# Performance work log

Measured on AMD Instinct MI355X. Metric: run time of the kernel, lower is better.

Reference implementation:

```python
import jax, jax.numpy as jnp
import numpy as np

L_LAYERS = 6   # decoder layers
N_HEAD = 8
NUM_PAIR = 100  # num_pair_queries
LN_EPS = 1e-5


def _ln(x, g, b):
    m = x.mean(-1, keepdims=True)
    v = ((x - m) ** 2).mean(-1, keepdims=True)
    return (x - m) / jnp.sqrt(v + LN_EPS) * g + b


def _mlp2(x, w1, b1, w2, b2):
    return jax.nn.relu(x @ w1.T + b1) @ w2.T + b2


def _mha(q, k, v, in_w, in_b, out_w, out_b):
    # torch nn.MultiheadAttention (batch_first, eval mode) equivalent
    C = q.shape[-1]
    dh = C // N_HEAD
    wq, wk, wv = jnp.split(in_w, 3, axis=0)
    bq, bk, bv = jnp.split(in_b, 3, axis=0)
    def heads(x, w, b):
        y = x @ w.T + b
        return y.reshape(x.shape[0], x.shape[1], N_HEAD, dh).transpose(0, 2, 1, 3)
    qh, kh, vh = heads(q, wq, bq), heads(k, wk, bk), heads(v, wv, bv)
    att = jax.nn.softmax(jnp.einsum('bhqd,bhkd->bhqk', qh, kh) * (1.0 / np.sqrt(dh)), axis=-1)
    out = jnp.einsum('bhqk,bhkd->bhqd', att, vh).transpose(0, 2, 1, 3).reshape(q.shape[0], q.shape[1], C)
    return out @ out_w.T + out_b


def reference(hs_last, mem, mem_pos, sub_boxes, obj_boxes,
              su_w1, su_b1, su_w2, su_b2, ou_w1, ou_b1, ou_w2, ou_b2,
              pm_w1, pm_b1, pm_w2, pm_b2, sp_w1, sp_b1, sp_w2, sp_b2,
              sa_in_w, sa_in_b, sa_out_w, sa_out_b, ca_in_w, ca_in_b, ca_out_w, ca_out_b,
              l1_w, l1_b, l2_w, l2_b, n1_g, n1_b, n2_g, n2_b, n3_g, n3_b):
    B, Q, C = hs_last.shape
    N = Q // 2
    hsp = hs_last.reshape(B, N, 2, C)
    sub_feat, obj_feat = hsp[:, :, 0, :], hsp[:, :, 1, :]

    # --- HumanObjectPairLearner.select_topk_indices (mapper='identity') ---
    sub_emb = _mlp2(sub_feat, su_w1, su_b1, su_w2, su_b2)
    obj_emb = _mlp2(obj_feat, ou_w1, ou_b1, ou_w2, ou_b2)
    sub_emb = sub_emb / (jnp.linalg.norm(sub_emb, axis=-1, keepdims=True) + 1e-6)
    obj_emb = obj_emb / (jnp.linalg.norm(obj_emb, axis=-1, keepdims=True) + 1e-6)
    importance = jnp.einsum('bnc,bmc->bnm', sub_emb, obj_emb)  # [B, N, N]
    K = min(NUM_PAIR, N * N)
    _, idx = jax.lax.top_k(importance.reshape(B, N * N), K)
    sub_pos, obj_pos = idx // N, idx % N  # [B, K]

    # --- build_pair_queries: gather selected sub/obj features ---
    sel_sub = jnp.take_along_axis(sub_feat, sub_pos[:, :, None], axis=1)  # [B, K, C]
    sel_obj = jnp.take_along_axis(obj_feat, obj_pos[:, :, None], axis=1)
    pair_q = _mlp2(jnp.concatenate([sel_sub, sel_obj], axis=-1), pm_w1, pm_b1, pm_w2, pm_b2)

    # --- PairSpatialEncoding ---
    sp = _mlp2(jnp.concatenate([sub_boxes, obj_boxes], axis=-1), sp_w1, sp_b1, sp_w2, sp_b2)

    # --- LocalityAwareInteractionDecoder (eval mode: dropout = identity) ---
    q = pair_q
    k_mem = mem + mem_pos
    for i in range(L_LAYERS):
        q_sp = q + sp
        sa = _mha(q_sp, q_sp, q_sp, sa_in_w[i], sa_in_b[i], sa_out_w[i], sa_out_b[i])
        q = _ln(q + sa, n1_g[i], n1_b[i])
        # original: cross_attn(cat([q, sp], dim=1), ...)[:, :K] -- attention is
        # per-query, so slicing after equals running cross-attn with q alone.
        ca = _mha(q, k_mem, mem, ca_in_w[i], ca_in_b[i], ca_out_w[i], ca_out_b[i])
        q = _ln(q + ca, n2_g[i], n2_b[i])
        ffn = jax.nn.relu(q @ l1_w[i].T + l1_b[i]) @ l2_w[i].T + l2_b[i]
        q = _ln(q + ffn, n3_g[i], n3_b[i])
    return q


def setup_inputs() -> dict:
    B, N, C, M, F, L = 32, 100, 256, 4096, 2048, L_LAYERS
    K = NUM_PAIR
    keys = iter(jax.random.split(jax.random.key(0), 80))
    def nrm(shape, s=1.0):
        return jax.random.normal(next(keys), shape, jnp.float32) * s
    w = lambda shape: nrm(shape, 0.02)
    return {
        'hs_last': nrm((B, 2 * N, C)),
        'mem': nrm((B, M, C)),
        'mem_pos': nrm((B, M, C)),
        'sub_boxes': jax.random.uniform(next(keys), (B, K, 4), jnp.float32),
        'obj_boxes': jax.random.uniform(next(keys), (B, K, 4), jnp.float32),
        'su_w1': w((C, C)), 'su_b1': jnp.zeros((C,)), 'su_w2': w((C, C)), 'su_b2': jnp.zeros((C,)),
        'ou_w1': w((C, C)), 'ou_b1': jnp.zeros((C,)), 'ou_w2': w((C, C)), 'ou_b2': jnp.zeros((C,)),
        'pm_w1': w((C, 2 * C)), 'pm_b1': jnp.zeros((C,)), 'pm_w2': w((C, C)), 'pm_b2': jnp.zeros((C,)),
        'sp_w1': w((C, 8)), 'sp_b1': jnp.zeros((C,)), 'sp_w2': w((C, C)), 'sp_b2': jnp.zeros((C,)),
        'sa_in_w': w((L, 3 * C, C)), 'sa_in_b': jnp.zeros((L, 3 * C)),
        'sa_out_w': w((L, C, C)), 'sa_out_b': jnp.zeros((L, C)),
        'ca_in_w': w((L, 3 * C, C)), 'ca_in_b': jnp.zeros((L, 3 * C)),
        'ca_out_w': w((L, C, C)), 'ca_out_b': jnp.zeros((L, C)),
        'l1_w': w((L, F, C)), 'l1_b': jnp.zeros((L, F)),
        'l2_w': w((L, C, F)), 'l2_b': jnp.zeros((L, C)),
        'n1_g': jnp.ones((L, C)), 'n1_b': jnp.zeros((L, C)),
        'n2_g': jnp.ones((L, C)), 'n2_b': jnp.zeros((L, C)),
        'n3_g': jnp.ones((L, C)), 'n3_b': jnp.zeros((L, C)),
    }
```

## Files before the change

### kernel.cpp

```cpp
#include <hip/hip_runtime.h>
#include <hip/hip_bf16.h>

#define Bb 32
#define Nn 100
#define Cc 256
#define Mm 4096
#define Ff 2048
#define Ll 6
#define Hh 8
#define DH 32
#define KP 100
#define TT (Bb*KP)
#define LNEPS 1e-5f
#define NCH 4
#define SUBK 128

typedef __hip_bfloat16 bf16;
typedef unsigned short ushort_t;
typedef __attribute__((ext_vector_type(8))) short short8v;
typedef __attribute__((ext_vector_type(4))) float f32x4;

union FragU { uint2 u2[2]; uint4 u4; short8v s8; };

__device__ __forceinline__ float bfu2f(unsigned short u) {
  union { unsigned u32; float f; } cv; cv.u32 = ((unsigned)u) << 16; return cv.f;
}
__device__ __forceinline__ unsigned short f2bf(float f) {
  union { float f; unsigned u; } c; c.f = f;
  unsigned r = c.u + 0x7FFF + ((c.u >> 16) & 1);
  return (unsigned short)(r >> 16);
}
__device__ __forceinline__ unsigned pack2(float a, float b) {
  return (unsigned)f2bf(a) | ((unsigned)f2bf(b) << 16);
}

template<int AT, bool RELU, int OM, bool PAIR>
__global__ __launch_bounds__(256) void gemm_mfma(
    const void* __restrict__ Av, const float* __restrict__ A2,
    const bf16* __restrict__ W, const float* __restrict__ bias,
    void* __restrict__ out,
    const void* __restrict__ Av2, const float* __restrict__ A2_2,
    const bf16* __restrict__ W2, const float* __restrict__ bias2,
    void* __restrict__ out2,
    int M, int N, int K)
{
  __shared__ ushort_t SM[2*128*72];
  ushort_t* As = SM;
  ushort_t* Bs = SM + 128*72;
  const int mt = M >> 7, nt = N >> 7;
  const int nwg1 = mt * nt;
  const int nwg = PAIR ? 2*nwg1 : nwg1;
  const int g = blockIdx.x;
  const int xcd = g & 7, lid = g >> 3;
  const int q8 = nwg >> 3, r8 = nwg & 7;
  int wgid = (xcd < r8 ? xcd*(q8+1) : r8*(q8+1) + (xcd - r8)*q8) + lid;
  if (PAIR && wgid >= nwg1) {
    wgid -= nwg1; Av = Av2; A2 = A2_2; W = W2; bias = bias2; out = out2;
  }
  const int ntile = wgid % nt, mtile = wgid / nt;
  const int bm = mtile << 7, bn = ntile << 7;
  const int tid = threadIdx.x;
  const int w = tid >> 6, lane = tid & 63;
  const int lr = lane & 15, lg = lane >> 4;
  const int wm = w >> 1, wn = w & 1;
  const float* Af = (const float*)Av;
  const bf16*  Ab = (const bf16*)Av;

  f32x4 acc[4][4] = {};

  for (int k0 = 0; k0 < K; k0 += 64) {
    __syncthreads();
    #pragma unroll
    for (int i = 0; i < 4; ++i) {
      int linear = i*256 + tid;
      int row = linear >> 3, c8 = linear & 7;
      uint4 packed;
      if (AT == 0) {
        const float* ap = Af + (size_t)(bm+row)*K + k0 + c8*8;
        float4 f0 = *(const float4*)ap;
        float4 f1 = *(const float4*)(ap+4);
        if (A2) {
          const float* ap2 = A2 + (size_t)(bm+row)*K + k0 + c8*8;
          float4 g0 = *(const float4*)ap2;
          float4 g1 = *(const float4*)(ap2+4);
          f0.x += g0.x; f0.y += g0.y; f0.z += g0.z; f0.w += g0.w;
          f1.x += g1.x; f1.y += g1.y; f1.z += g1.z; f1.w += g1.w;
        }
        packed.x = pack2(f0.x, f0.y); packed.y = pack2(f0.z, f0.w);
        packed.z = pack2(f1.x, f1.y); packed.w = pack2(f1.z, f1.w);
      } else {
        packed = *(const uint4*)(Ab + (size_t)(bm+row)*K + k0 + c8*8);
      }
      *(uint4*)&As[row*72 + c8*8] = packed;
      uint4 wb = *(const uint4*)(W + (size_t)(bn+row)*K + k0 + c8*8);
      *(uint4*)&Bs[row*72 + c8*8] = wb;
    }
    __syncthreads();
    #pragma unroll
    for (int kk = 0; kk < 64; kk += 32) {
      FragU a[4];
      #pragma unroll
      for (int mi = 0; mi < 4; ++mi)
        a[mi].u4 = *(const uint4*)&As[(wm*64 + mi*16 + lr)*72 + kk + lg*8];
      #pragma unroll
      for (int ni = 0; ni < 4; ++ni) {
        FragU bfr;
        bfr.u4 = *(const uint4*)&Bs[(wn*64 + ni*16 + lr)*72 + kk + lg*8];
        #pragma unroll
        for (int mi = 0; mi < 4; ++mi)
          acc[mi][ni] = __builtin_amdgcn_mfma_f32_16x16x32_bf16(a[mi].s8, bfr.s8,
                                                                acc[mi][ni], 0, 0, 0);
      }
    }
  }

  if (OM == 2) {
    __syncthreads();
    ushort_t* Ct = SM;
    #pragma unroll
    for (int ni = 0; ni < 4; ++ni) {
      int col = wn*64 + ni*16 + lr;
      float bv = bias[bn + col];
      #pragma unroll
      for (int mi = 0; mi < 4; ++mi)
        #pragma unroll
        for (int r = 0; r < 4; ++r) {
          int rowl = wm*64 + mi*16 + lg*4 + r;
          Ct[rowl*136 + col] = f2bf(acc[mi][ni][r] + bv);
        }
    }
    __syncthreads();
    for (int u = tid; u < 2048; u += 256) {
      int rowl = u >> 4, sub = u & 15;
      uint4 v = *(const uint4*)&Ct[rowl*136 + sub*8];
      int m = bm + rowl;
      int gcol = bn + sub*8;
      int bb = m >> 12, mm = m & 4095;
      int h = gcol >> 5, dd = gcol & 31;
      *(uint4*)((bf16*)out + (((size_t)bb*Hh + h)*Mm + mm)*DH + dd) = v;
    }
  } else {
    #pragma unroll
    for (int ni = 0; ni < 4; ++ni) {
      int col = bn + wn*64 + ni*16 + lr;
      float bv = bias ? bias[col] : 0.f;
      #pragma unroll
      for (int mi = 0; mi < 4; ++mi) {
        #pragma unroll
        for (int r = 0; r < 4; ++r) {
          int m = bm + wm*64 + mi*16 + lg*4 + r;
          float v = acc[mi][ni][r] + bv;
          if (RELU) v = fmaxf(v, 0.f);
          if (OM == 0) {
            ((float*)out)[(size_t)m*N + col] = v;
          } else if (OM == 1) {
            ((bf16*)out)[(size_t)m*N + col] = __float2bfloat16(v);
          } else {
            int bb = m / KP, qq = m % KP;
            int h = col >> 5, dd = col & 31;
            ((bf16*)out)[(((size_t)bb*Hh + h)*KP + qq)*DH + dd] =
                __float2bfloat16(v * 0.17677669529663687f);
          }
        }
      }
    }
  }
}

template<int AT>
__global__ __launch_bounds__(512) void gemm_ln(
    const void* __restrict__ Av, const bf16* __restrict__ W,
    const float* __restrict__ bias, const float* __restrict__ resid,
    const float* __restrict__ gamma, const float* __restrict__ beta,
    float* __restrict__ out, int M, int K,
    const bf16* __restrict__ part, const float2* __restrict__ ml)
{
  __shared__ ushort_t As[16][72];
  __shared__ ushort_t Bs[256][72];
  __shared__ float redS[16][8];
  __shared__ float redQ[16][8];
  const int bm = blockIdx.x * 16;
  const int tid = threadIdx.x;
  const int w = tid >> 6, lane = tid & 63;
  const int lr = lane & 15, lg = lane >> 4;
  const float* Af = (const float*)Av;
  const bf16*  Ab = (const bf16*)Av;
  f32x4 acc[2] = {};

  for (int k0 = 0; k0 < K; k0 += 64) {
    __syncthreads();
    if (tid < 128) {
      int row = tid >> 3, c8 = tid & 7;
      uint4 packed;
      if (AT == 0) {
        const float* ap = Af + (size_t)(bm+row)*K + k0 + c8*8;
        float4 f0 = *(const float4*)ap;
        float4 f1 = *(const float4*)(ap+4);
        packed.x = pack2(f0.x, f0.y); packed.y = pack2(f0.z, f0.w);
        packed.z = pack2(f1.x, f1.y); packed.w = pack2(f1.z, f1.w);
      } else if (AT == 1) {
        packed = *(const uint4*)(Ab + (size_t)(bm+row)*K + k0 + c8*8);
      } else {
        int t = bm + row;
        int b = t / KP, q = t % KP;
        int ch0 = k0 + c8*8;
        int h = ch0 >> 5, d0 = ch0 & 31;
        int bh = b*Hh + h;
        float2 m0 = ml[((size_t)bh*NCH + 0)*KP + q];
        float2 m1 = ml[((size_t)bh*NCH + 1)*KP + q];
        float2 m2 = ml[((size_t)bh*NCH + 2)*KP + q];
        float2 m3 = ml[((size_t)bh*NCH + 3)*KP + q];
        float mm = fmaxf(fmaxf(m0.x, m1.x), fmaxf(m2.x, m3.x));
        float w0 = __expf(m0.x - mm), w1 = __expf(m1.x - mm);
        float w2 = __expf(m2.x - mm), w3 = __expf(m3.x - mm);
        float invL = 1.f / (m0.y*w0 + m1.y*w1 + m2.y*w2 + m3.y*w3);
        float o[8] = {};
        float wc[NCH] = { w0, w1, w2, w3 };
        #pragma unroll
        for (int c = 0; c < NCH; ++c) {
          uint4 pv = *(const uint4*)(part + (((size_t)bh*NCH + c)*KP + q)*DH + d0);
          const ushort_t* pe = (const ushort_t*)&pv;
          #pragma unroll
          for (int e = 0; e < 8; ++e) o[e] += wc[c] * bfu2f(pe[e]);
        }
        packed.x = pack2(o[0]*invL, o[1]*invL);
        packed.y = pack2(o[2]*invL, o[3]*invL);
        packed.z = pack2(o[4]*invL, o[5]*invL);
        packed.w = pack2(o[6]*invL, o[7]*invL);
      }
      *(uint4*)&As[row][c8*8] = packed;
    }
    #pragma unroll
    for (int i = 0; i < 4; ++i) {
      int linear = i*512 + tid;
      int row = linear >> 3, c8 = linear & 7;
      *(uint4*)&Bs[row][c8*8] = *(const uint4*)(W + (size_t)row*K + k0 + c8*8);
    }
    __syncthreads();
    #pragma unroll
    for (int kk = 0; kk < 64; kk += 32) {
      FragU a;
      a.u4 = *(const uint4*)&As[lr][kk + lg*8];
      #pragma unroll
      for (int ni = 0; ni < 2; ++ni) {
        FragU bfr;
        bfr.u4 = *(const uint4*)&Bs[w*32 + ni*16 + lr][kk + lg*8];
        acc[ni] = __builtin_amdgcn_mfma_f32_16x16x32_bf16(a.s8, bfr.s8, acc[ni], 0, 0, 0);
      }
    }
  }

  float x[2][4];
  #pragma unroll
  for (int r = 0; r < 4; ++r) {
    int row = bm + lg*4 + r;
    float s = 0.f, sq = 0.f;
    #pragma unroll
    for (int ni = 0; ni < 2; ++ni) {
      int col = w*32 + ni*16 + lr;
      float v = acc[ni][r] + bias[col] + resid[(size_t)row*Cc + col];
      x[ni][r] = v;
      s += v; sq += v*v;
    }
    #pragma unroll
    for (int m2 = 1; m2 < 16; m2 <<= 1) { s += __shfl_xor(s, m2); sq += __shfl_xor(sq, m2); }
    if (lr == 0) { redS[lg*4 + r][w] = s; redQ[lg*4 + r][w] = sq; }
  }
  __syncthreads();
  #pragma unroll
  for (int r = 0; r < 4; ++r) {
    int lrow = lg*4 + r;
    float ss = 0.f, sq = 0.f;
    #pragma unroll
    for (int j = 0; j < 8; ++j) { ss += redS[lrow][j]; sq += redQ[lrow][j]; }
    float mean = ss * (1.f/Cc);
    float var = sq * (1.f/Cc) - mean*mean;
    float inv = rsqrtf(var + LNEPS);
    #pragma unroll
    for (int ni = 0; ni < 2; ++ni) {
      int col = w*32 + ni*16 + lr;
      out[(size_t)(bm+lrow)*Cc + col] = (x[ni][r] - mean)*inv*gamma[col] + beta[col];
    }
  }
}

#define NSEG 8
struct CvtDesc {
  const float* src[NSEG];
  bf16* dst[NSEG];
  int n4[NSEG];
  int total4;
};
__global__ __launch_bounds__(256) void cvt_multi(CvtDesc d) {
  int stride = gridDim.x * blockDim.x;
  for (int i = blockIdx.x*256 + threadIdx.x; i < d.total4; i += stride) {
    int seg = 0, off = i;
    while (off >= d.n4[seg]) { off -= d.n4[seg]; ++seg; }
    float4 f = *(const float4*)(d.src[seg] + (size_t)off*4);
    uint2 p; p.x = pack2(f.x, f.y); p.y = pack2(f.z, f.w);
    *(uint2*)(d.dst[seg] + (size_t)off*4) = p;
  }
}

__global__ __launch_bounds__(256) void prep_mem(const float* __restrict__ mem,
                                                const float* __restrict__ mem_pos,
                                                bf16* __restrict__ kb, bf16* __restrict__ vb,
                                                int n16) {
  int i = blockIdx.x*256 + threadIdx.x;
  if (i >= n16) return;
  size_t base = (size_t)i * 16;
  float4 a[4], p[4];
  #pragma unroll
  for (int t = 0; t < 4; ++t) {
    a[t] = *(const float4*)(mem + base + t*4);
    p[t] = *(const float4*)(mem_pos + base + t*4);
  }
  #pragma unroll
  for (int h = 0; h < 2; ++h) {
    uint4 vv, kv;
    vv.x = pack2(a[2*h].x, a[2*h].y);     vv.y = pack2(a[2*h].z, a[2*h].w);
    vv.z = pack2(a[2*h+1].x, a[2*h+1].y); vv.w = pack2(a[2*h+1].z, a[2*h+1].w);
    kv.x = pack2(a[2*h].x + p[2*h].x,     a[2*h].y + p[2*h].y);
    kv.y = pack2(a[2*h].z + p[2*h].z,     a[2*h].w + p[2*h].w);
    kv.z = pack2(a[2*h+1].x + p[2*h+1].x, a[2*h+1].y + p[2*h+1].y);
    kv.w = pack2(a[2*h+1].z + p[2*h+1].z, a[2*h+1].w + p[2*h+1].w);
    *(uint4*)(vb + base + h*8) = vv;
    *(uint4*)(kb + base + h*8) = kv;
  }
}

template<bool RELU>
__global__ __launch_bounds__(256) void gemm_nt(
    const float* __restrict__ A0, const float* __restrict__ W0,
    const float* __restrict__ b0, float* __restrict__ o0,
    const float* __restrict__ A1, const float* __restrict__ W1,
    const float* __restrict__ b1, float* __restrict__ o1,
    int M, int N, int K)
{
  const float* A = blockIdx.z ? A1 : A0;
  const float* Wt = blockIdx.z ? W1 : W0;
  const float* bias = blockIdx.z ? b1 : b0;
  float* out = blockIdx.z ? o1 : o0;
  __shared__ float As[16][68];
  __shared__ float Ws[16][68];
  const int bm = blockIdx.y * 64, bn = blockIdx.x * 64;
  const int tid = threadIdx.x;
  const int kk = tid & 15, rr = tid >> 4;
  const int tx = tid & 15, ty = tid >> 4;
  float acc[4][4] = {};
  for (int k0 = 0; k0 < K; k0 += 16) {
    #pragma unroll
    for (int p = 0; p < 4; ++p) {
      int m = rr + p*16;
      int row = bm + m;
      float av = 0.f, wv = 0.f;
      bool kin = (k0 + kk) < K;
      if (row < M && kin) av = A[(size_t)row * K + k0 + kk];
      int wrow = bn + m;
      if (wrow < N && kin) wv = Wt[(size_t)wrow * K + k0 + kk];
      As[kk][m] = av;
      Ws[kk][m] = wv;
    }
    __syncthreads();
    #pragma unroll
    for (int q = 0; q < 16; ++q) {
      float a[4], w[4];
      #pragma unroll
      for (int i = 0; i < 4; ++i) a[i] = As[q][ty*4 + i];
      #pragma unroll
      for (int j = 0; j < 4; ++j) w[j] = Ws[q][tx*4 + j];
      #pragma unroll
      for (int i = 0; i < 4; ++i)
        #pragma unroll
        for (int j = 0; j < 4; ++j) acc[i][j] += a[i] * w[j];
    }
    __syncthreads();
  }
  #pragma unroll
  for (int i = 0; i < 4; ++i) {
    int row = bm + ty*4 + i;
    if (row >= M) continue;
    #pragma unroll
    for (int j = 0; j < 4; ++j) {
      int col = bn + tx*4 + j;
      if (col >= N) continue;
      float v = acc[i][j];
      if (bias) v += bias[col];
      if (RELU) v = v > 0.f ? v : 0.f;
      out[(size_t)row*N + col] = v;
    }
  }
}

__global__ void split_subobj(const float* __restrict__ hs,
                             float* __restrict__ subf, float* __restrict__ objf) {
  int i = blockIdx.x*256 + threadIdx.x;
  if (i >= Bb*Nn*Cc) return;
  int c = i % Cc, n = (i / Cc) % Nn, b = i / (Cc*Nn);
  subf[i] = hs[((size_t)b*2*Nn + 2*n    )*Cc + c];
  objf[i] = hs[((size_t)b*2*Nn + 2*n + 1)*Cc + c];
}

__global__ __launch_bounds__(256) void l2norm_kernel(float* __restrict__ x) {
  int t = blockIdx.x, c = threadIdx.x;
  float v = x[(size_t)t*Cc + c];
  __shared__ float red[256];
  red[c] = v*v; __syncthreads();
  for (int s = 128; s > 0; s >>= 1) { if (c < s) red[c] += red[c+s]; __syncthreads(); }
  float scale = 1.f / (sqrtf(red[0]) + 1e-6f);
  x[(size_t)t*Cc + c] = v * scale;
}

__global__ __launch_bounds__(128) void importance_kernel(const float* __restrict__ se,
                                                         const float* __restrict__ oe,
                                                         float* __restrict__ imp) {
  int b = blockIdx.x / Nn, n = blockIdx.x % Nn;
  int m = threadIdx.x;
  if (m >= Nn) return;
  const float* s = se + ((size_t)b*Nn + n)*Cc;
  const float* o = oe + ((size_t)b*Nn + m)*Cc;
  float acc = 0.f;
  for (int c = 0; c < Cc; ++c) acc += s[c] * o[c];
  imp[((size_t)b*Nn + n)*Nn + m] = acc;
}

__global__ __launch_bounds__(1024) void topk_kernel(const float* __restrict__ imp,
                                                    int* __restrict__ idx_out) {
  __shared__ unsigned mu[Nn*Nn];
  __shared__ unsigned hist[256];
  __shared__ unsigned prefix;
  __shared__ int remK;
  __shared__ unsigned long long keys[128];
  __shared__ unsigned tiebuf[256];
  __shared__ unsigned cnt_gt, cnt_tie;
  const int b = blockIdx.x, tid = threadIdx.x;
  const int NN = Nn*Nn;

  for (int i = tid; i < NN; i += 1024) {
    unsigned u = __float_as_uint(imp[(size_t)b*NN + i]);
    mu[i] = (u & 0x80000000u) ? ~u : (u | 0x80000000u);
  }
  if (tid == 0) { prefix = 0u; remK = KP; cnt_gt = 0u; cnt_tie = 0u; }
  __syncthreads();

  for (int shift = 24; shift >= 0; shift -= 8) {
    if (tid < 256) hist[tid] = 0u;
    __syncthreads();
    unsigned pmask = (shift == 24) ? 0u : (0xFFFFFFFFu << (shift + 8));
    unsigned pref = prefix;
    for (int i = tid; i < NN; i += 1024) {
      unsigned v = mu[i];
      if ((v & pmask) == pref) atomicAdd(&hist[(v >> shift) & 0xFFu], 1u);
    }
    __syncthreads();
    if (tid == 0) {
      int rk = remK;
      unsigned sel = 0u;
      for (int bin = 255; bin >= 0; --bin) {
        int c = (int)hist[bin];
        if (c >= rk) { sel = (unsigned)bin; break; }
        rk -= c;
      }
      remK = rk;
      prefix = pref | (sel << shift);
    }
    __syncthreads();
  }

  const unsigned T = prefix;
  const int need = remK;

  for (int i = tid; i < NN; i += 1024) {
    unsigned v = mu[i];
    if (v > T) {
      unsigned p = atomicAdd(&cnt_gt, 1u);
      keys[p] = ((unsigned long long)(~v) << 32) | (unsigned)i;
    } else if (v == T) {
      unsigned p = atomicAdd(&cnt_tie, 1u);
      if (p < 256u) tiebuf[p] = (unsigned)i;
    }
  }
  __syncthreads();
  const unsigned ngt = cnt_gt;
  const unsigned nt_ = cnt_tie < 256u ? cnt_tie : 256u;

  for (int i = tid; i < 256; i += 1024) if (i >= (int)nt_) tiebuf[i] = 0xFFFFFFFFu;
  __syncthreads();
  for (int ksz = 2; ksz <= 256; ksz <<= 1) {
    for (int st = ksz >> 1; st > 0; st >>= 1) {
      if (tid < 128) {
        int i = ((tid & ~(st-1)) << 1) | (tid & (st-1));
        int j = i | st;
        bool up = ((i & ksz) == 0);
        unsigned a = tiebuf[i], c = tiebuf[j];
        if ((a > c) == up) { tiebuf[i] = c; tiebuf[j] = a; }
      }
      __syncthreads();
    }
  }
  for (int t = tid; t < need; t += 1024)
    keys[ngt + t] = ((unsigned long long)(~T) << 32) | tiebuf[t];
  for (int i = tid; i < 128; i += 1024)
    if (i >= KP) keys[i] = 0xFFFFFFFFFFFFFFFFull;
  __syncthreads();

  for (int ksz = 2; ksz <= 128; ksz <<= 1) {
    for (int st = ksz >> 1; st > 0; st >>= 1) {
      if (tid < 64) {
        int i = ((tid & ~(st-1)) << 1) | (tid & (st-1));
        int j = i | st;
        bool up = ((i & ksz) == 0);
        unsigned long long a = keys[i], c = keys[j];
        if ((a > c) == up) { keys[i] = c; keys[j] = a; }
      }
      __syncthreads();
    }
  }
  if (tid < KP) idx_out[b*KP + tid] = (int)(keys[tid] & 0xFFFFFFFFu);
}

__global__ __launch_bounds__(256) void gather_pair(const float* __restrict__ subf,
                                                   const float* __restrict__ objf,
                                                   const int* __restrict__ idx,
                                                   float* __restrict__ pc) {
  int bk = blockIdx.x;
  int b = bk / KP;
  int id = idx[bk];
  int spos = id / Nn, opos = id % Nn;
  const float* s = subf + ((size_t)b*Nn + spos)*Cc;
  const float* o = objf + ((size_t)b*Nn + opos)*Cc;
  float* dst = pc + (size_t)bk * (2*Cc);
  for (int c = threadIdx.x; c < Cc; c += 256) { dst[c] = s[c]; dst[Cc + c] = o[c]; }
}

__global__ void boxes_cat_kernel(const float* __restrict__ sb, const float* __restrict__ ob,
                                 float* __restrict__ out) {
  int i = blockIdx.x*256 + threadIdx.x;
  if (i >= TT*8) return;
  int c = i & 7, bk = i >> 3;
  out[i] = (c < 4) ? sb[bk*4 + c] : ob[bk*4 + (c - 4)];
}

__global__ __launch_bounds__(512) void attn_sa(const bf16* __restrict__ qkv,
                                               float* __restrict__ out) {
  __shared__ float Kt[128][36];
  __shared__ float Vt[128][36];
  __shared__ float Qs[KP][DH];
  __shared__ float Ps[8][128];
  int bh = blockIdx.x; int b = bh >> 3, h = bh & 7;
  int tid = threadIdx.x;
  const float scale = 0.17677669529663687f;
  const size_t base = (size_t)b * KP * (3*Cc);
  for (int i = tid; i < KP*DH; i += 512) {
    int q = i >> 5, d = i & 31;
    Qs[q][d] = __bfloat162float(qkv[base + (size_t)q*(3*Cc) + h*DH + d]) * scale;
  }
  {
    int j = tid >> 2, qc = tid & 3;
    float kf[8], vf[8];
    if (j < KP) {
      uint4 kraw = *(const uint4*)(qkv + base + (size_t)j*(3*Cc) + Cc   + h*DH + qc*8);
      uint4 vraw = *(const uint4*)(qkv + base + (size_t)j*(3*Cc) + 2*Cc + h*DH + qc*8);
      const ushort_t* ks = (const ushort_t*)&kraw;
      const ushort_t* vs = (const ushort_t*)&vraw;
      #pragma unroll
      for (int e = 0; e < 8; ++e) { kf[e] = bfu2f(ks[e]); vf[e] = bfu2f(vs[e]); }
    } else {
      #pragma unroll
      for (int e = 0; e < 8; ++e) { kf[e] = 0.f; vf[e] = 0.f; }
    }
    ((float4*)Kt[j])[qc*2]   = make_float4(kf[0],kf[1],kf[2],kf[3]);
    ((float4*)Kt[j])[qc*2+1] = make_float4(kf[4],kf[5],kf[6],kf[7]);
    ((float4*)Vt[j])[qc*2]   = make_float4(vf[0],vf[1],vf[2],vf[3]);
    ((float4*)Vt[j])[qc*2+1] = make_float4(vf[4],vf[5],vf[6],vf[7]);
  }
  __syncthreads();
  int w = tid >> 6, lane = tid & 63;
  int d = lane & 31, half = lane >> 5;
  for (int q = w; q < KP; q += 8) {
    float s0 = 0.f, s1 = 0.f;
    #pragma unroll
    for (int c = 0; c < 8; ++c) {
      float4 k0 = ((const float4*)Kt[lane])[c];
      float4 k1 = ((const float4*)Kt[lane+64])[c];
      float4 qv = *(const float4*)&Qs[q][c*4];
      s0 += k0.x*qv.x + k0.y*qv.y + k0.z*qv.z + k0.w*qv.w;
      s1 += k1.x*qv.x + k1.y*qv.y + k1.z*qv.z + k1.w*qv.w;
    }
    if (lane >= KP) s0 = -1e30f;
    if (lane + 64 >= KP) s1 = -1e30f;
    float mx = fmaxf(s0, s1);
    #pragma unroll
    for (int m2 = 32; m2 > 0; m2 >>= 1) mx = fmaxf(mx, __shfl_xor(mx, m2));
    float p0 = (lane < KP)      ? expf(s0 - mx) : 0.f;
    float p1 = (lane + 64 < KP) ? expf(s1 - mx) : 0.f;
    float sm = p0 + p1;
    #pragma unroll
    for (int m2 = 32; m2 > 0; m2 >>= 1) sm += __shfl_xor(sm, m2);
    Ps[w][lane] = p0; Ps[w][lane+64] = p1;
    float pv = 0.f;
    for (int s = 0; s < 64; ++s) {
      int j = half*64 + s;
      pv += Ps[w][j] * Vt[j][d];
    }
    pv += __shfl_xor(pv, 32);
    if (lane < 32) out[((size_t)b*KP + q)*Cc + h*DH + d] = pv / sm;
  }
}

__global__ __launch_bounds__(256) void attn_ca_mfma(
    const bf16* __restrict__ qhH,
    const bf16* __restrict__ khH,
    const bf16* __restrict__ vhH,
    bf16* __restrict__ part,
    float2* __restrict__ ml)
{
  __shared__ unsigned short Vs[32][140];
  const int bx = blockIdx.x;
  const int bh = bx >> 2, ch = bx & 3;
  const int tid = threadIdx.x;
  const int w = tid >> 6, lane = tid & 63;
  const int lr = lane & 15, lg = lane >> 4;
  const int k0base = ch * (Mm / NCH);
  const int qt0 = w, qt1 = w + 4;

  FragU qf[2];
  {
    int r0 = qt0*16 + lr;
    qf[0].u4 = *(const uint4*)(qhH + ((size_t)bh*KP + r0)*DH + lg*8);
    int r1 = qt1*16 + lr;
    if (r1 < KP) qf[1].u4 = *(const uint4*)(qhH + ((size_t)bh*KP + r1)*DH + lg*8);
    else         qf[1].u4 = make_uint4(0u,0u,0u,0u);
  }

  f32x4 acc[2][2] = {};
  float mreg[2] = {-1e30f, -1e30f};
  float lreg[2] = {0.f, 0.f};

  const int srcA = (2*(lg & 1))*16 + lr;
  const int srcB = srcA + 16;
  const bool hi_kt = (lg >> 1) != 0;

  for (int sc = 0; sc < (Mm/NCH)/SUBK; ++sc) {
    const int k0 = k0base + sc*SUBK;
    __syncthreads();
    {
      int p2 = tid & 63, c = tid >> 6;
      uint4 v0 = *(const uint4*)(vhH + ((size_t)bh*Mm + k0 + 2*p2    )*DH + c*8);
      uint4 v1 = *(const uint4*)(vhH + ((size_t)bh*Mm + k0 + 2*p2 + 1)*DH + c*8);
      const unsigned short* a0 = (const unsigned short*)&v0;
      const unsigned short* a1 = (const unsigned short*)&v1;
      #pragma unroll
      for (int e = 0; e < 8; ++e) {
        int d = c*8 + e;
        *(unsigned int*)&Vs[d][2*p2] = (unsigned)a0[e] | ((unsigned)a1[e] << 16);
      }
    }
    FragU kf[8];
    #pragma unroll
    for (int kt = 0; kt < 8; ++kt)
      kf[kt].u4 = *(const uint4*)(khH + ((size_t)bh*Mm + k0 + kt*16 + lr)*DH + lg*8);
    __syncthreads();

    #pragma unroll
    for (int j = 0; j < 2; ++j) {
      f32x4 sv[8];
      #pragma unroll
      for (int kt = 0; kt < 8; ++kt) {
        f32x4 z = {0.f, 0.f, 0.f, 0.f};
        sv[kt] = __builtin_amdgcn_mfma_f32_16x16x32_bf16(kf[kt].s8, qf[j].s8, z, 0, 0, 0);
      }
      float mx = -1e30f;
      #pragma unroll
      for (int kt = 0; kt < 8; ++kt)
        mx = fmaxf(mx, fmaxf(fmaxf(sv[kt][0], sv[kt][1]), fmaxf(sv[kt][2], sv[kt][3])));
      mx = fmaxf(mx, __shfl_xor(mx, 16));
      mx = fmaxf(mx, __shfl_xor(mx, 32));
      float newm = fmaxf(mreg[j], mx);
      float resc = __expf(mreg[j] - newm);
      mreg[j] = newm;
      float psum = 0.f;
      unsigned pl[8], ph[8];
      #pragma unroll
      for (int kt = 0; kt < 8; ++kt) {
        float p0 = __expf(sv[kt][0] - newm);
        float p1 = __expf(sv[kt][1] - newm);
        float p2 = __expf(sv[kt][2] - newm);
        float p3 = __expf(sv[kt][3] - newm);
        psum += (p0 + p1) + (p2 + p3);
        pl[kt] = pack2(p0, p1);
        ph[kt] = pack2(p2, p3);
      }
      psum += __shfl_xor(psum, 16);
      psum += __shfl_xor(psum, 32);
      lreg[j] = lreg[j]*resc + psum;
      #pragma unroll
      for (int dt = 0; dt < 2; ++dt)
        #pragma unroll
        for (int r = 0; r < 4; ++r) acc[j][dt][r] *= resc;

      #pragma unroll
      for (int ks = 0; ks < 4; ++ks) {
        unsigned aA = __shfl(pl[2*ks],   srcA), bA = __shfl(pl[2*ks+1], srcA);
        unsigned aB = __shfl(ph[2*ks],   srcA), bB = __shfl(ph[2*ks+1], srcA);
        unsigned cA = __shfl(pl[2*ks],   srcB), dA = __shfl(pl[2*ks+1], srcB);
        unsigned cB = __shfl(ph[2*ks],   srcB), dB = __shfl(ph[2*ks+1], srcB);
        FragU pf;
        pf.u4.x = hi_kt ? bA : aA;
        pf.u4.y = hi_kt ? bB : aB;
        pf.u4.z = hi_kt ? dA : cA;
        pf.u4.w = hi_kt ? dB : cB;
        #pragma unroll
        for (int dt = 0; dt < 2; ++dt) {
          FragU vf;
          vf.u2[0] = *(const uint2*)&Vs[dt*16 + lr][ks*32 + lg*8];
          vf.u2[1] = *(const uint2*)&Vs[dt*16 + lr][ks*32 + lg*8 + 4];
          acc[j][dt] = __builtin_amdgcn_mfma_f32_16x16x32_bf16(vf.s8, pf.s8,
                                                               acc[j][dt], 0, 0, 0);
        }
      }
    }
  }

  #pragma unroll
  for (int j = 0; j < 2; ++j) {
    int q = (j ? qt1 : qt0)*16 + lr;
    if (q < KP) {
      if (lg == 0) ml[((size_t)bh*NCH + ch)*KP + q] = make_float2(mreg[j], lreg[j]);
      #pragma unroll
      for (int dt = 0; dt < 2; ++dt)
        #pragma unroll
        for (int r = 0; r < 4; ++r) {
          int d = dt*16 + lg*4 + r;
          part[(((size_t)bh*NCH + ch)*KP + q)*DH + d] = __float2bfloat16(acc[j][dt][r]);
        }
    }
  }
}

extern "C" void kernel_launch(void* const* d_in, const int* in_sizes, int n_in,
                              void* d_out, int out_size, void* d_ws, size_t ws_size,
                              hipStream_t stream) {
  auto in = [&](int i) { return (const float*)d_in[i]; };
  const float* hs        = in(0);
  const float* mem       = in(1);
  const float* mem_pos   = in(2);
  const float* sub_boxes = in(3);
  const float* obj_boxes = in(4);
  const float* su_w1 = in(5),  *su_b1 = in(6),  *su_w2 = in(7),  *su_b2 = in(8);
  const float* ou_w1 = in(9),  *ou_b1 = in(10), *ou_w2 = in(11), *ou_b2 = in(12);
  const float* pm_w1 = in(13), *pm_b1 = in(14), *pm_w2 = in(15), *pm_b2 = in(16);
  const float* sp_w1 = in(17), *sp_b1 = in(18), *sp_w2 = in(19), *sp_b2 = in(20);
  const float* sa_in_w = in(21),  *sa_in_b = in(22), *sa_out_w = in(23), *sa_out_b = in(24);
  const float* ca_in_w = in(25),  *ca_in_b = in(26), *ca_out_w = in(27), *ca_out_b = in(28);
  const float* l1_w = in(29), *l1_b = in(30), *l2_w = in(31), *l2_b = in(32);
  const float* n1_g = in(33), *n1_b = in(34), *n2_g = in(35), *n2_b = in(36);
  const float* n3_g = in(37), *n3_b = in(38);

  char* wsp = (char*)d_ws;
  auto alloc = [&](size_t bytes) { char* p = wsp; wsp += (bytes + 255) & ~(size_t)255; return p; };
  bf16* khH = (bf16*)alloc((size_t)Bb*Mm*Cc*2);
  bf16* vhH = (bf16*)alloc((size_t)Bb*Mm*Cc*2);
  bf16* kmem_b = (bf16*)alloc((size_t)Bb*Mm*Cc*2);
  bf16* vmem_b = (bf16*)alloc((size_t)Bb*Mm*Cc*2);
  bf16* qhH = (bf16*)alloc((size_t)TT*Cc*2);
  bf16* part = (bf16*)alloc((size_t)Bb*Hh*NCH*KP*DH*2);
  float2* mlbuf = (float2*)alloc((size_t)Bb*Hh*NCH*KP*8);
  bf16* sawb = (bf16*)alloc((size_t)Ll*3*Cc*Cc*2);
  bf16* cawb = (bf16*)alloc((size_t)Ll*3*Cc*Cc*2);
  bf16* sowb = (bf16*)alloc((size_t)Ll*Cc*Cc*2);
  bf16* cowb = (bf16*)alloc((size_t)Ll*Cc*Cc*2);
  bf16* l1wb = (bf16*)alloc((size_t)Ll*Ff*Cc*2);
  bf16* l2wb = (bf16*)alloc((size_t)Ll*Cc*Ff*2);
  bf16* pm1b = (bf16*)alloc((size_t)Cc*2*Cc*2);
  bf16* pm2b = (bf16*)alloc((size_t)Cc*Cc*2);
  float* subf    = (float*)alloc((size_t)Bb*Nn*Cc*4);
  float* objf    = (float*)alloc((size_t)Bb*Nn*Cc*4);
  float* sub_emb = (float*)alloc((size_t)Bb*Nn*Cc*4);
  float* obj_emb = (float*)alloc((size_t)Bb*Nn*Cc*4);
  float* embh    = (float*)alloc((size_t)TT*2*Cc*4);
  float* embh2   = (float*)alloc((size_t)TT*Cc*4);
  float* imp     = (float*)alloc((size_t)Bb*Nn*Nn*4);
  int*   idx     = (int*)  alloc((size_t)Bb*KP*4);
  float* pair_cat= (float*)alloc((size_t)TT*2*Cc*4);
  float* bxc     = (float*)alloc((size_t)TT*8*4);
  float* spb     = (float*)alloc((size_t)TT*Cc*4);
  float* qbuf    = (float*)alloc((size_t)TT*Cc*4);
  bf16*  qkvb    = (bf16*)alloc((size_t)TT*3*Cc*2);
  float* attn_o  = (float*)alloc((size_t)TT*Cc*4);
  bf16*  ffnb    = (bf16*)alloc((size_t)TT*Ff*2);

  {
    CvtDesc d;
    const float* srcs[NSEG] = { sa_in_w, ca_in_w, sa_out_w, ca_out_w, l1_w, l2_w, pm_w1, pm_w2 };
    bf16* dsts[NSEG] = { sawb, cawb, sowb, cowb, l1wb, l2wb, pm1b, pm2b };
    size_t ns[NSEG] = { (size_t)Ll*3*Cc*Cc, (size_t)Ll*3*Cc*Cc, (size_t)Ll*Cc*Cc,
                        (size_t)Ll*Cc*Cc, (size_t)Ll*Ff*Cc, (size_t)Ll*Cc*Ff,
                        (size_t)Cc*2*Cc, (size_t)Cc*Cc };
    int tot = 0;
    for (int i = 0; i < NSEG; ++i) { d.src[i] = srcs[i]; d.dst[i] = dsts[i]; d.n4[i] = (int)(ns[i]/4); tot += d.n4[i]; }
    d.total4 = tot;
    cvt_multi<<<2048, 256, 0, stream>>>(d);
  }
  {
    int n16 = (int)((size_t)Bb*Mm*Cc/16);
    prep_mem<<<(n16 + 255)/256, 256, 0, stream>>>(mem, mem_pos, kmem_b, vmem_b, n16);
  }

  auto GFP = [&](const float* A0, const float* W0, const float* b0, float* o0,
                 const float* A1, const float* W1, const float* b1, float* o1,
                 int M, int N, int K, bool relu, int zz) {
    dim3 g((N + 63)/64, (M + 63)/64, zz), t(256);
    if (relu) gemm_nt<true ><<<g, t, 0, stream>>>(A0,W0,b0,o0,A1,W1,b1,o1,M,N,K);
    else      gemm_nt<false><<<g, t, 0, stream>>>(A0,W0,b0,o0,A1,W1,b1,o1,M,N,K);
  };

  auto GM = [&](const void* A, const float* A2, const bf16* W, const float* bias,
                void* out, int M, int N, int K, int OM, bool relu) {
    int blocks = (M >> 7) * (N >> 7);
    if (OM == 0) {
      if (relu) gemm_mfma<0,true ,0,false><<<blocks,256,0,stream>>>(A,A2,W,bias,out,nullptr,nullptr,nullptr,nullptr,nullptr,M,N,K);
      else      gemm_mfma<0,false,0,false><<<blocks,256,0,stream>>>(A,A2,W,bias,out,nullptr,nullptr,nullptr,nullptr,nullptr,M,N,K);
    } else if (OM == 1) {
      if (relu) gemm_mfma<0,true ,1,false><<<blocks,256,0,stream>>>(A,A2,W,bias,out,nullptr,nullptr,nullptr,nullptr,nullptr,M,N,K);
      else      gemm_mfma<0,false,1,false><<<blocks,256,0,stream>>>(A,A2,W,bias,out,nullptr,nullptr,nullptr,nullptr,nullptr,M,N,K);
    } else {
      gemm_mfma<0,false,3,false><<<blocks,256,0,stream>>>(A,A2,W,bias,out,nullptr,nullptr,nullptr,nullptr,nullptr,M,N,K);
    }
  };

  split_subobj<<<(Bb*Nn*Cc + 255)/256, 256, 0, stream>>>(hs, subf, objf);
  GFP(subf, su_w1, su_b1, embh,  objf,  ou_w1, ou_b1, embh2, TT, Cc, Cc, true,  2);
  GFP(embh, su_w2, su_b2, sub_emb, embh2, ou_w2, ou_b2, obj_emb, TT, Cc, Cc, false, 2);
  l2norm_kernel<<<2*TT, 256, 0, stream>>>(sub_emb);
  importance_kernel<<<Bb*Nn, 128, 0, stream>>>(sub_emb, obj_emb, imp);
  topk_kernel<<<Bb, 1024, 0, stream>>>(imp, idx);
  gather_pair<<<TT, 256, 0, stream>>>(subf, objf, idx, pair_cat);
  GM(pair_cat, nullptr, pm1b, pm_b1, embh, TT, Cc, 2*Cc, 0, true);
  GM(embh,     nullptr, pm2b, pm_b2, qbuf, TT, Cc, Cc,   0, false);
  boxes_cat_kernel<<<(TT*8 + 255)/256, 256, 0, stream>>>(sub_boxes, obj_boxes, bxc);
  GFP(bxc,  sp_w1, sp_b1, embh, nullptr,nullptr,nullptr,nullptr, TT, Cc, 8,  true,  1);
  GFP(embh, sp_w2, sp_b2, spb,  nullptr,nullptr,nullptr,nullptr, TT, Cc, Cc, false, 1);

  for (int i = 0; i < Ll; ++i) {
    const bf16* sawL = sawb + (size_t)i*3*Cc*Cc;
    const bf16* cawL = cawb + (size_t)i*3*Cc*Cc;
    const float* sab = sa_in_b + (size_t)i*3*Cc;
    const float* cab = ca_in_b + (size_t)i*3*Cc;

    GM(qbuf, spb, sawL, sab, qkvb, TT, 3*Cc, Cc, 1, false);
    attn_sa<<<Bb*Hh, 512, 0, stream>>>(qkvb, attn_o);
    gemm_ln<0><<<TT/16, 512, 0, stream>>>(attn_o, sowb + (size_t)i*Cc*Cc,
        sa_out_b + (size_t)i*Cc, qbuf, n1_g + i*Cc, n1_b + i*Cc, qbuf, TT, Cc,
        nullptr, nullptr);

    GM(qbuf, nullptr, cawL, cab, qhH, TT, Cc, Cc, 3, false);
    {
      int blocks = 2 * ((Bb*Mm) >> 7) * (Cc >> 7);
      gemm_mfma<1,false,2,true><<<blocks, 256, 0, stream>>>(
          kmem_b, nullptr, cawL + (size_t)Cc*Cc, cab + Cc, khH,
          vmem_b, nullptr, cawL + (size_t)2*Cc*Cc, cab + 2*Cc, vhH, Bb*Mm, Cc, Cc);
    }
    attn_ca_mfma<<<Bb*Hh*NCH, 256, 0, stream>>>(qhH, khH, vhH, part, mlbuf);
    gemm_ln<2><<<TT/16, 512, 0, stream>>>(nullptr, cowb + (size_t)i*Cc*Cc,
        ca_out_b + (size_t)i*Cc, qbuf, n2_g + i*Cc, n2_b + i*Cc, qbuf, TT, Cc,
        part, mlbuf);

    GM(qbuf, nullptr, l1wb + (size_t)i*Ff*Cc, l1_b + (size_t)i*Ff, ffnb, TT, Ff, Cc, 1, true);
    float* qo = (i == Ll-1) ? (float*)d_out : qbuf;
    gemm_ln<1><<<TT/16, 512, 0, stream>>>(ffnb, l2wb + (size_t)i*Cc*Ff,
        l2_b + (size_t)i*Cc, qbuf, n3_g + i*Cc, n3_b + i*Cc, qo, TT, Ff,
        nullptr, nullptr);
  }
}
```

Before: 1.974 ms.

## Batch cross-attention K/V projections across layers reading fp32 memory directly

When workspace allows, the K/V projections for several decoder layers are computed in one wide GEMM per group of layers. That GEMM reads the fp32 memory and positional tensors directly, so the bf16 prep_mem pass is skipped, and its results go into per-layer slots. The aim is to read the large memory tensor once per group instead of once per layer and to drop the separate conversion pass. In exchange it needs much more workspace, up to six layers of K/V, and it falls back to the old path if the workspace is too small.

```diff
diff --git a/kernel.cpp b/kernel.cpp
--- a/kernel.cpp
+++ b/kernel.cpp
@@ -114,13 +114,14 @@
     }
   }
 
-  if (OM == 2) {
+  if (OM == 2 || OM == 4) {
     __syncthreads();
     ushort_t* Ct = SM;
     #pragma unroll
     for (int ni = 0; ni < 4; ++ni) {
+      int colg = bn + wn*64 + ni*16 + lr;
+      float bv = (OM == 4) ? bias[(colg >> 8)*(3*Cc) + (colg & 255)] : bias[colg];
       int col = wn*64 + ni*16 + lr;
-      float bv = bias[bn + col];
       #pragma unroll
       for (int mi = 0; mi < 4; ++mi)
         #pragma unroll
@@ -136,8 +137,14 @@
       int m = bm + rowl;
       int gcol = bn + sub*8;
       int bb = m >> 12, mm = m & 4095;
-      int h = gcol >> 5, dd = gcol & 31;
-      *(uint4*)((bf16*)out + (((size_t)bb*Hh + h)*Mm + mm)*DH + dd) = v;
+      if (OM == 2) {
+        int h = gcol >> 5, dd = gcol & 31;
+        *(uint4*)((bf16*)out + (((size_t)bb*Hh + h)*Mm + mm)*DH + dd) = v;
+      } else {
+        int slot = gcol >> 8, h = (gcol >> 5) & 7, dd = gcol & 31;
+        *(uint4*)((bf16*)out +
+            (((size_t)(slot*Bb + bb)*Hh + h)*Mm + mm)*DH + dd) = v;
+      }
     }
   } else {
     #pragma unroll
@@ -284,7 +291,7 @@
   }
 }
 
-#define NSEG 8
+#define NSEG 20
 struct CvtDesc {
   const float* src[NSEG];
   bf16* dst[NSEG];
@@ -759,10 +766,6 @@
 
   char* wsp = (char*)d_ws;
   auto alloc = [&](size_t bytes) { char* p = wsp; wsp += (bytes + 255) & ~(size_t)255; return p; };
-  bf16* khH = (bf16*)alloc((size_t)Bb*Mm*Cc*2);
-  bf16* vhH = (bf16*)alloc((size_t)Bb*Mm*Cc*2);
-  bf16* kmem_b = (bf16*)alloc((size_t)Bb*Mm*Cc*2);
-  bf16* vmem_b = (bf16*)alloc((size_t)Bb*Mm*Cc*2);
   bf16* qhH = (bf16*)alloc((size_t)TT*Cc*2);
   bf16* part = (bf16*)alloc((size_t)Bb*Hh*NCH*KP*DH*2);
   float2* mlbuf = (float2*)alloc((size_t)Bb*Hh*NCH*KP*8);
@@ -774,6 +777,8 @@
   bf16* l2wb = (bf16*)alloc((size_t)Ll*Cc*Ff*2);
   bf16* pm1b = (bf16*)alloc((size_t)Cc*2*Cc*2);
   bf16* pm2b = (bf16*)alloc((size_t)Cc*Cc*2);
+  bf16* kwAll = (bf16*)alloc((size_t)Ll*Cc*Cc*2);
+  bf16* vwAll = (bf16*)alloc((size_t)Ll*Cc*Cc*2);
   float* subf    = (float*)alloc((size_t)Bb*Nn*Cc*4);
   float* objf    = (float*)alloc((size_t)Bb*Nn*Cc*4);
   float* sub_emb = (float*)alloc((size_t)Bb*Nn*Cc*4);
@@ -790,19 +795,51 @@
   float* attn_o  = (float*)alloc((size_t)TT*Cc*4);
   bf16*  ffnb    = (bf16*)alloc((size_t)TT*Ff*2);
 
+  const size_t layerKV = (size_t)Bb*Hh*Mm*DH*2;
+  size_t used = (size_t)(wsp - (char*)d_ws);
+  size_t rem = (ws_size > used) ? ws_size - used : 0;
+  int S = 0;
+  if (rem > (32u<<20)) S = (int)((rem - (32u<<20)) / (2*layerKV));
+  if (S > 6) S = 6;
+  int NL;
+  bool modeA = (S >= 2);
+  bf16 *khAll=nullptr, *vhAll=nullptr, *kmem_b=nullptr, *vmem_b=nullptr;
+  if (modeA) {
+    NL = (S >= 6) ? 6 : (S >= 3) ? 3 : 2;
+    khAll = (bf16*)alloc((size_t)NL*layerKV);
+    vhAll = (bf16*)alloc((size_t)NL*layerKV);
+  } else {
+    NL = 1;
+    khAll = (bf16*)alloc(layerKV);
+    vhAll = (bf16*)alloc(layerKV);
+    kmem_b = (bf16*)alloc(layerKV);
+    vmem_b = (bf16*)alloc(layerKV);
+  }
+
   {
     CvtDesc d;
-    const float* srcs[NSEG] = { sa_in_w, ca_in_w, sa_out_w, ca_out_w, l1_w, l2_w, pm_w1, pm_w2 };
-    bf16* dsts[NSEG] = { sawb, cawb, sowb, cowb, l1wb, l2wb, pm1b, pm2b };
-    size_t ns[NSEG] = { (size_t)Ll*3*Cc*Cc, (size_t)Ll*3*Cc*Cc, (size_t)Ll*Cc*Cc,
-                        (size_t)Ll*Cc*Cc, (size_t)Ll*Ff*Cc, (size_t)Ll*Cc*Ff,
-                        (size_t)Cc*2*Cc, (size_t)Cc*Cc };
+    int s = 0;
+    auto seg = [&](const float* src, bf16* dst, size_t n) {
+      d.src[s] = src; d.dst[s] = dst; d.n4[s] = (int)(n/4); ++s;
+    };
+    seg(sa_in_w, sawb, (size_t)Ll*3*Cc*Cc);
+    seg(ca_in_w, cawb, (size_t)Ll*3*Cc*Cc);
+    seg(sa_out_w, sowb, (size_t)Ll*Cc*Cc);
+    seg(ca_out_w, cowb, (size_t)Ll*Cc*Cc);
+    seg(l1_w, l1wb, (size_t)Ll*Ff*Cc);
+    seg(l2_w, l2wb, (size_t)Ll*Cc*Ff);
+    seg(pm_w1, pm1b, (size_t)Cc*2*Cc);
+    seg(pm_w2, pm2b, (size_t)Cc*Cc);
+    for (int i = 0; i < Ll; ++i)
+      seg(ca_in_w + (size_t)i*3*Cc*Cc + (size_t)Cc*Cc,   kwAll + (size_t)i*Cc*Cc, (size_t)Cc*Cc);
+    for (int i = 0; i < Ll; ++i)
+      seg(ca_in_w + (size_t)i*3*Cc*Cc + (size_t)2*Cc*Cc, vwAll + (size_t)i*Cc*Cc, (size_t)Cc*Cc);
     int tot = 0;
-    for (int i = 0; i < NSEG; ++i) { d.src[i] = srcs[i]; d.dst[i] = dsts[i]; d.n4[i] = (int)(ns[i]/4); tot += d.n4[i]; }
+    for (int i = 0; i < NSEG; ++i) tot += d.n4[i];
     d.total4 = tot;
     cvt_multi<<<2048, 256, 0, stream>>>(d);
   }
-  {
+  if (!modeA) {
     int n16 = (int)((size_t)Bb*Mm*Cc/16);
     prep_mem<<<(n16 + 255)/256, 256, 0, stream>>>(mem, mem_pos, kmem_b, vmem_b, n16);
   }
@@ -848,6 +885,16 @@
     const float* sab = sa_in_b + (size_t)i*3*Cc;
     const float* cab = ca_in_b + (size_t)i*3*Cc;
 
+    if (modeA && (i % NL) == 0) {
+      int Npass = NL * Cc;
+      int blocks = 2 * ((Bb*Mm) >> 7) * (Npass >> 7);
+      gemm_mfma<0,false,4,true><<<blocks, 256, 0, stream>>>(
+          mem, mem_pos, kwAll + (size_t)i*Cc*Cc,
+          ca_in_b + (size_t)i*3*Cc + Cc,   khAll,
+          mem, nullptr,  vwAll + (size_t)i*Cc*Cc,
+          ca_in_b + (size_t)i*3*Cc + 2*Cc, vhAll, Bb*Mm, Npass, Cc);
+    }
+
     GM(qbuf, spb, sawL, sab, qkvb, TT, 3*Cc, Cc, 1, false);
     attn_sa<<<Bb*Hh, 512, 0, stream>>>(qkvb, attn_o);
     gemm_ln<0><<<TT/16, 512, 0, stream>>>(attn_o, sowb + (size_t)i*Cc*Cc,
@@ -855,13 +902,19 @@
         nullptr, nullptr);
 
     GM(qbuf, nullptr, cawL, cab, qhH, TT, Cc, Cc, 3, false);
-    {
+    const bf16 *khL, *vhL;
+    if (modeA) {
+      int slot = i % NL;
+      khL = khAll + (size_t)slot*Bb*Hh*Mm*DH;
+      vhL = vhAll + (size_t)slot*Bb*Hh*Mm*DH;
+    } else {
       int blocks = 2 * ((Bb*Mm) >> 7) * (Cc >> 7);
       gemm_mfma<1,false,2,true><<<blocks, 256, 0, stream>>>(
-          kmem_b, nullptr, cawL + (size_t)Cc*Cc, cab + Cc, khH,
-          vmem_b, nullptr, cawL + (size_t)2*Cc*Cc, cab + 2*Cc, vhH, Bb*Mm, Cc, Cc);
-    }
-    attn_ca_mfma<<<Bb*Hh*NCH, 256, 0, stream>>>(qhH, khH, vhH, part, mlbuf);
+          kmem_b, nullptr, cawL + (size_t)Cc*Cc, cab + Cc, khAll,
+          vmem_b, nullptr, cawL + (size_t)2*Cc*Cc, cab + 2*Cc, vhAll, Bb*Mm, Cc, Cc);
+      khL = khAll; vhL = vhAll;
+    }
+    attn_ca_mfma<<<Bb*Hh*NCH, 256, 0, stream>>>(qhH, khL, vhL, part, mlbuf);
     gemm_ln<2><<<TT/16, 512, 0, stream>>>(nullptr, cowb + (size_t)i*Cc*Cc,
         ca_out_b + (size_t)i*Cc, qbuf, n2_g + i*Cc, n2_b + i*Cc, qbuf, TT, Cc,
         part, mlbuf);
```

Result: slower. 2.191 ms (+11.0%).
